# Kernel tuning notes

Measured on AMD Instinct MI355X. Metric: run time of the kernel, lower is better.

## Reference

```python
import jax, jax.numpy as jnp
import numpy as np

N_NODES = 40000
N_EDGES = 640000
N_GRAPHS = 64
D_IN = 128
D_H = 128
N_LAYERS = 3
EPS = 1e-5


def _layer_norm(x, g, b):
    mu = jnp.mean(x, axis=-1, keepdims=True)
    var = jnp.var(x, axis=-1, keepdims=True)
    return (x - mu) * jax.lax.rsqrt(var + EPS) * g + b


def _sage_conv(x, src, dst, Wl, bl, Wr):
    # mean aggregation of neighbor messages: i <- mean_{j: (j->i)} x_j
    msg = x[src]                                              # [E, d]
    agg = jax.ops.segment_sum(msg, dst, num_segments=N_NODES)  # [N, d]
    deg = jax.ops.segment_sum(jnp.ones((src.shape[0],), x.dtype), dst,
                              num_segments=N_NODES)
    agg = agg / jnp.clip(deg, 1.0)[:, None]
    # out = lin_l(agg) + lin_r(x)
    return agg @ Wl.T + bl + x @ Wr.T


def setup_inputs() -> dict:
    key = jax.random.key(0)
    ks = jax.random.split(key, 12)
    s = 0.05
    x = jax.random.normal(ks[0], (N_NODES, D_IN), jnp.float32)
    edge_index = jax.random.randint(ks[1], (2, N_EDGES), 0, N_NODES, jnp.int64)
    batch = jnp.sort(jax.random.randint(ks[2], (N_NODES,), 0, N_GRAPHS, jnp.int64))
    fc_w = jax.random.normal(ks[3], (D_H, D_IN), jnp.float32) * s
    fc_b = jax.random.normal(ks[4], (D_H,), jnp.float32) * s
    Wl = jax.random.normal(ks[5], (N_LAYERS, D_H, D_H), jnp.float32) * s
    bl = jax.random.normal(ks[6], (N_LAYERS, D_H), jnp.float32) * s
    Wr = jax.random.normal(ks[7], (N_LAYERS, D_H, D_H), jnp.float32) * s
    ln_g = jnp.ones((N_LAYERS - 1, D_H), jnp.float32)
    ln_b = jnp.zeros((N_LAYERS - 1, D_H), jnp.float32)
    return {"x": x, "edge_index": edge_index, "batch": batch,
            "fc_w": fc_w, "fc_b": fc_b, "Wl": Wl, "bl": bl, "Wr": Wr,
            "ln_g": ln_g, "ln_b": ln_b}


def reference(x, edge_index, batch, fc_w, fc_b, Wl, bl, Wr, ln_g, ln_b):
    src, dst = edge_index[0], edge_index[1]
    # input projection + ReLU
    h = jax.nn.relu(x @ fc_w.T + fc_b)
    # GraphSAGE stack: norm + ReLU between layers, none after the last
    for i in range(N_LAYERS):
        h = _sage_conv(h, src, dst, Wl[i], bl[i], Wr[i])
        if i < N_LAYERS - 1:
            h = jax.nn.relu(_layer_norm(h, ln_g[i], ln_b[i]))
    node_embed = h                                            # [N, D_H]
    graph_embed = jax.ops.segment_sum(node_embed, batch,
                                      num_segments=N_GRAPHS)  # [G, D_H]
    return node_embed, graph_embed
```

## Files before the change

### kernel.cpp

```cpp
#include <hip/hip_runtime.h>
#include <hip/hip_bf16.h>


#define N_NODES 40000
#define N_EDGES 640000
#define N_GRAPHS 64
#define D 128
#define NODE_ELEMS 5120000
#define N_TILES 1250
#define ELL_W 64

typedef __hip_bfloat16 bf16;
typedef __attribute__((ext_vector_type(8))) short bf16x8;
typedef __attribute__((ext_vector_type(4))) float f32x4;

__device__ __forceinline__ float b2f(bf16 v) { return __bfloat162float(v); }
__device__ __forceinline__ bf16 f2b(float v) { return __float2bfloat16(v); }
__device__ __forceinline__ float lo2f(unsigned w) { return __uint_as_float(w << 16); }
__device__ __forceinline__ float hi2f(unsigned w) { return __uint_as_float(w & 0xffff0000u); }
__device__ __forceinline__ unsigned packbf(float a, float b) {
    union { bf16 h[2]; unsigned u; } c;
    c.h[0] = f2b(a); c.h[1] = f2b(b);
    return c.u;
}
__device__ __forceinline__ int is_bf16(const unsigned* lng) {
    return (lng[0] == 0x3f803f80u) ? 1 : 0;
}
__device__ __forceinline__ int edge_is_i64(const void* edge) {
    const unsigned* ew = (const unsigned*)edge;
    return (ew[1] == 0u && ew[3] == 0u && ew[5] == 0u) ? 1 : 0;
}

union U8 { uint4 u; bf16x8 s; };

__device__ __forceinline__ bf16x8 load8(const void* base, long idx, int isb) {
    if (isb) {
        U8 t;
        t.u = *(const uint4*)((const bf16*)base + idx);
        return t.s;
    }
    const float* f = (const float*)base + idx;
    float4 f0 = *(const float4*)f;
    float4 f1 = *(const float4*)(f + 4);
    union { bf16 h[8]; bf16x8 s; } t;
    t.h[0] = f2b(f0.x); t.h[1] = f2b(f0.y); t.h[2] = f2b(f0.z); t.h[3] = f2b(f0.w);
    t.h[4] = f2b(f1.x); t.h[5] = f2b(f1.y); t.h[6] = f2b(f1.z); t.h[7] = f2b(f1.w);
    return t.s;
}

#define CW2_TOTAL 99200
__global__ __launch_bounds__(256, 2) void k_main(
    const void* __restrict__ X, const void* __restrict__ fcw,
    const void* __restrict__ fcb, bf16* __restrict__ outb,
    const void* __restrict__ edge, const void* __restrict__ batch,
    const void* Wl, const void* bl, const void* Wr,
    const void* lng, const void* lnb,
    int* __restrict__ cursor, unsigned short* __restrict__ ell,
    int* __restrict__ batch32, bf16* __restrict__ cw,
    float* __restrict__ gsum) {
    const int bid = blockIdx.x, t = threadIdx.x;
    int role, id;
    if (bid < 1000) { role = (bid & 1) ? 0 : 1; id = bid >> 1; }
    else if (bid < 1012) { role = 0; id = 500 + (bid - 1000); }
    else if (bid < 1169) { role = 2; id = bid - 1012; }
    else { role = 3; id = bid - 1169; }

    if (role == 1) {
        const int i64 = edge_is_i64(edge);
        int s[5], d[5];
#pragma unroll
        for (int i = 0; i < 5; i++) {
            int e = id * 1280 + i * 256 + t;
            if (i64) {
                s[i] = (int)((const long long*)edge)[e];
                d[i] = (int)((const long long*)edge)[N_EDGES + e];
            } else {
                s[i] = ((const int*)edge)[e];
                d[i] = ((const int*)edge)[N_EDGES + e];
            }
        }
        int p[5];
#pragma unroll
        for (int i = 0; i < 5; i++) p[i] = atomicAdd(&cursor[d[i]], 1);
#pragma unroll
        for (int i = 0; i < 5; i++)
            if (p[i] < ELL_W) ell[d[i] * ELL_W + p[i]] = (unsigned short)s[i];
        return;
    }
    if (role == 2) {
        int j = id * 256 + t;
        if (j < N_NODES)
            batch32[j] = edge_is_i64(edge) ? (int)((const long long*)batch)[j]
                                           : ((const int*)batch)[j];
        return;
    }
    if (role == 3) {
        int i = id * 256 + t;
        if (i >= CW2_TOTAL) return;
        int isb = is_bf16((const unsigned*)lng);
        const void* s; int o;
        if (i < 49152)       { s = Wl;  o = i; }
        else if (i < 49536)  { s = bl;  o = i - 49152; }
        else if (i < 98688)  { s = Wr;  o = i - 49536; }
        else if (i < 98944)  { s = lng; o = i - 98688; }
        else                 { s = lnb; o = i - 98944; }
        cw[i] = isb ? ((const bf16*)s)[o] : f2b(((const float*)s)[o]);
        return;
    }

    {
        int i = id * 256 + t;
        if (i < N_GRAPHS * D) gsum[i] = 0.f;
    }
    const int lane = t & 63;
    const int wave = t >> 6;
    const int n = lane & 15, q = lane >> 4;
    const int rowgrp = wave >> 1;
    const int cb = (wave & 1) * 64;
    const int isb = is_bf16((const unsigned*)lng);

    bf16x8 wf[4][4];
#pragma unroll
    for (int ct = 0; ct < 4; ct++)
#pragma unroll
        for (int ks = 0; ks < 4; ks++)
            wf[ct][ks] = load8(fcw, (long)(cb + ct * 16 + n) * 128 + ks * 32 + q * 8, isb);
    float bz[4];
#pragma unroll
    for (int ct = 0; ct < 4; ct++)
        bz[ct] = isb ? b2f(((const bf16*)fcb)[cb + ct * 16 + n])
                     : ((const float*)fcb)[cb + ct * 16 + n];

    const f32x4 zero = {0.f, 0.f, 0.f, 0.f};
    for (int tile = id; tile < N_TILES; tile += 512) {
        const long rbase = (long)tile * 32 + rowgrp * 16 + n;
        f32x4 acc[4] = {zero, zero, zero, zero};
        bf16x8 af[4];
#pragma unroll
        for (int ks = 0; ks < 4; ks++)
            af[ks] = load8(X, rbase * 128 + ks * 32 + q * 8, isb);
#pragma unroll
        for (int ct = 0; ct < 4; ct++)
#pragma unroll
            for (int ks = 0; ks < 4; ks++)
                acc[ct] = __builtin_amdgcn_mfma_f32_16x16x32_bf16(
                    af[ks], wf[ct][ks], acc[ct], 0, 0, 0);
#pragma unroll
        for (int ct = 0; ct < 4; ct++) {
            const int col = cb + ct * 16 + n;
#pragma unroll
            for (int r = 0; r < 4; r++) {
                const long row = (long)tile * 32 + rowgrp * 16 + q * 4 + r;
                outb[row * 128 + col] = f2b(fmaxf(acc[ct][r] + bz[ct], 0.f));
            }
        }
    }
}

__global__ void k_agg(const bf16* __restrict__ h, const int* __restrict__ cursor,
                      const unsigned short* __restrict__ ell, bf16* __restrict__ agg) {
    const int node = blockIdx.x * 16 + (threadIdx.x >> 4);
    const int l16 = threadIdx.x & 15;
    const int deg = min(cursor[node], ELL_W);
    const int dm1 = max(deg - 1, 0);
    const unsigned short* row = ell + node * ELL_W;
    const uint4* hp = (const uint4*)h;
    float a0 = 0.f, a1 = 0.f, a2 = 0.f, a3 = 0.f;
    float a4 = 0.f, a5 = 0.f, a6 = 0.f, a7 = 0.f;
    for (int e = 0; e < deg; e += 8) {
#pragma unroll
        for (int i = 0; i < 8; i++) {
            int ei = min(e + i, dm1);
            int idx = (int)row[ei];
            uint4 w = hp[(size_t)idx * 16 + l16];
            float m = (e + i < deg) ? 1.f : 0.f;
            a0 = fmaf(m, lo2f(w.x), a0); a1 = fmaf(m, hi2f(w.x), a1);
            a2 = fmaf(m, lo2f(w.y), a2); a3 = fmaf(m, hi2f(w.y), a3);
            a4 = fmaf(m, lo2f(w.z), a4); a5 = fmaf(m, hi2f(w.z), a5);
            a6 = fmaf(m, lo2f(w.w), a6); a7 = fmaf(m, hi2f(w.w), a7);
        }
    }
    float inv = 1.f / (float)max(deg, 1);
    uint4 o;
    o.x = packbf(a0 * inv, a1 * inv);
    o.y = packbf(a2 * inv, a3 * inv);
    o.z = packbf(a4 * inv, a5 * inv);
    o.w = packbf(a6 * inv, a7 * inv);
    ((uint4*)agg)[(size_t)node * 16 + l16] = o;
}

template <int MODE>
__global__ __launch_bounds__(256, 2) void k_gemm(
    const bf16* __restrict__ A, const bf16* __restrict__ W1,
    const bf16* __restrict__ B, const bf16* __restrict__ W2,
    const bf16* __restrict__ bias, bf16* __restrict__ outb,
    void* __restrict__ outx, const bf16* __restrict__ lgam,
    const bf16* __restrict__ lbet, const unsigned* __restrict__ lngraw) {
    __shared__ float sred[2][2][16][2];
    const int tid = threadIdx.x;
    const int lane = tid & 63;
    const int wave = tid >> 6;
    const int n = lane & 15, q = lane >> 4;
    const int rowgrp = wave >> 1;
    const int cbi = wave & 1;
    const int cb = cbi * 64;
    const int isb = is_bf16(lngraw);

    bf16x8 wf[2][4][4];
#pragma unroll
    for (int p = 0; p < 2; p++) {
        const bf16* Wp = p ? W2 : W1;
#pragma unroll
        for (int ct = 0; ct < 4; ct++)
#pragma unroll
            for (int ks = 0; ks < 4; ks++) {
                U8 t;
                t.u = *(const uint4*)&Wp[(cb + ct * 16 + n) * 128 + ks * 32 + q * 8];
                wf[p][ct][ks] = t.s;
            }
    }
    float bz[4], gf[4], bf_[4];
#pragma unroll
    for (int ct = 0; ct < 4; ct++) {
        bz[ct] = b2f(bias[cb + ct * 16 + n]);
        if (MODE == 1) {
            gf[ct] = b2f(lgam[cb + ct * 16 + n]);
            bf_[ct] = b2f(lbet[cb + ct * 16 + n]);
        }
    }

    const f32x4 zero = {0.f, 0.f, 0.f, 0.f};

    for (int tile = blockIdx.x; tile < N_TILES; tile += gridDim.x) {
        const long rbase = (long)tile * 32 + rowgrp * 16 + n;
        f32x4 acc[4] = {zero, zero, zero, zero};
#pragma unroll
        for (int p = 0; p < 2; p++) {
            const bf16* Ap = p ? B : A;
            bf16x8 af[4];
#pragma unroll
            for (int ks = 0; ks < 4; ks++) {
                U8 t;
                t.u = *(const uint4*)&Ap[rbase * 128 + ks * 32 + q * 8];
                af[ks] = t.s;
            }
#pragma unroll
            for (int ct = 0; ct < 4; ct++)
#pragma unroll
                for (int ks = 0; ks < 4; ks++)
                    acc[ct] = __builtin_amdgcn_mfma_f32_16x16x32_bf16(
                        af[ks], wf[p][ct][ks], acc[ct], 0, 0, 0);
        }

        float vs[4][4];
#pragma unroll
        for (int ct = 0; ct < 4; ct++)
#pragma unroll
            for (int r = 0; r < 4; r++) vs[ct][r] = acc[ct][r] + bz[ct];

        if (MODE == 1) {
            float s[4], ss[4];
#pragma unroll
            for (int r = 0; r < 4; r++) {
                s[r] = 0.f; ss[r] = 0.f;
#pragma unroll
                for (int ct = 0; ct < 4; ct++) {
                    s[r] += vs[ct][r];
                    ss[r] += vs[ct][r] * vs[ct][r];
                }
            }
#pragma unroll
            for (int m = 1; m <= 8; m <<= 1)
#pragma unroll
                for (int r = 0; r < 4; r++) {
                    s[r] += __shfl_xor(s[r], m, 64);
                    ss[r] += __shfl_xor(ss[r], m, 64);
                }
            if (n == 0) {
#pragma unroll
                for (int r = 0; r < 4; r++) {
                    sred[rowgrp][cbi][q * 4 + r][0] = s[r];
                    sred[rowgrp][cbi][q * 4 + r][1] = ss[r];
                }
            }
            __syncthreads();
#pragma unroll
            for (int r = 0; r < 4; r++) {
                float S = s[r] + sred[rowgrp][1 - cbi][q * 4 + r][0];
                float SS = ss[r] + sred[rowgrp][1 - cbi][q * 4 + r][1];
                float mu = S * (1.f / 128.f);
                float var = SS * (1.f / 128.f) - mu * mu;
                float rstd = rsqrtf(var + 1e-5f);
#pragma unroll
                for (int ct = 0; ct < 4; ct++)
                    vs[ct][r] = fmaxf((vs[ct][r] - mu) * rstd * gf[ct] + bf_[ct], 0.f);
            }
            __syncthreads();
        }

#pragma unroll
        for (int ct = 0; ct < 4; ct++) {
            const int col = cb + ct * 16 + n;
#pragma unroll
            for (int r = 0; r < 4; r++) {
                const long row = (long)tile * 32 + rowgrp * 16 + q * 4 + r;
                float v = vs[ct][r];
                if (MODE == 1) {
                    outb[row * 128 + col] = f2b(v);
                } else {
                    if (isb) ((bf16*)outx)[row * 128 + col] = f2b(v);
                    else ((float*)outx)[row * 128 + col] = v;
                }
            }
        }
    }
}

__device__ __forceinline__ int lbound(const int* a, int n, int key) {
    int lo = 0, hi = n;
    while (lo < hi) {
        int mid = (lo + hi) >> 1;
        if (a[mid] < key) lo = mid + 1; else hi = mid;
    }
    return lo;
}

__global__ void k_graph(const void* __restrict__ node, const int* __restrict__ batch,
                        float* __restrict__ gsum, const unsigned* __restrict__ lngraw) {
    const int g = blockIdx.x >> 4, part = blockIdx.x & 15;
    const int c = threadIdx.x;
    const int isb = is_bf16(lngraw);
    const int lo = lbound(batch, N_NODES, g);
    const int hi = lbound(batch, N_NODES, g + 1);
    const int len = hi - lo;
    const int b0 = lo + (len * part) / 16;
    const int b1 = lo + (len * (part + 1)) / 16;
    float s0 = 0.f, s1 = 0.f;
    int n = b0;
    if (isb) {
        const bf16* nb = (const bf16*)node;
        for (; n + 2 <= b1; n += 2) {
            s0 += b2f(nb[(size_t)(n + 0) * 128 + c]);
            s1 += b2f(nb[(size_t)(n + 1) * 128 + c]);
        }
        for (; n < b1; n++) s0 += b2f(nb[(size_t)n * 128 + c]);
    } else {
        const float* nf = (const float*)node;
        for (; n + 2 <= b1; n += 2) {
            s0 += nf[(size_t)(n + 0) * 128 + c];
            s1 += nf[(size_t)(n + 1) * 128 + c];
        }
        for (; n < b1; n++) s0 += nf[(size_t)n * 128 + c];
    }
    atomicAdd(&gsum[g * 128 + c], s0 + s1);
}

__global__ void k_gout(const float* __restrict__ gsum, void* __restrict__ out,
                       const unsigned* __restrict__ lngraw) {
    int i = blockIdx.x * 256 + threadIdx.x;
    if (i >= N_GRAPHS * D) return;
    if (is_bf16(lngraw)) ((bf16*)out)[NODE_ELEMS + i] = f2b(gsum[i]);
    else ((float*)out)[NODE_ELEMS + i] = gsum[i];
}

extern "C" void kernel_launch(void* const* d_in, const int* in_sizes, int n_in,
                              void* d_out, int out_size, void* d_ws, size_t ws_size,
                              hipStream_t stream) {
    const void* x = d_in[0];
    const void* edge = d_in[1];
    const void* batch = d_in[2];
    const void* fc_w = d_in[3];
    const void* fc_b = d_in[4];
    const void* Wl = d_in[5];
    const void* bl = d_in[6];
    const void* Wr = d_in[7];
    const void* ln_g = d_in[8];
    const void* ln_b = d_in[9];
    const unsigned* lngraw = (const unsigned*)ln_g;

    size_t off = 0;
    char* base = (char*)d_ws;
    auto carve = [&](size_t bytes) -> char* {
        char* p = base + off;
        off = (off + bytes + 255) & ~(size_t)255;
        return p;
    };
    bf16* cw = (bf16*)carve((size_t)CW2_TOTAL * 2);
    bf16* hA = (bf16*)carve((size_t)NODE_ELEMS * 2);
    bf16* hB = (bf16*)carve((size_t)NODE_ELEMS * 2);
    bf16* agg = (bf16*)carve((size_t)NODE_ELEMS * 2);
    int* batch32 = (int*)carve((size_t)N_NODES * 4);
    unsigned short* ell = (unsigned short*)carve((size_t)N_NODES * ELL_W * 2);
    int* cursor = (int*)carve((size_t)N_NODES * 4);
    float* gsum = (float*)carve((size_t)N_GRAPHS * D * 4);

    const bf16* cw_Wl = cw;
    const bf16* cw_bl = cw + 49152;
    const bf16* cw_Wr = cw + 49536;
    const bf16* cw_lng = cw + 98688;
    const bf16* cw_lnb = cw + 98944;

    hipMemsetAsync(cursor, 0, (size_t)N_NODES * 4, stream);
    k_main<<<1557, 256, 0, stream>>>(x, fc_w, fc_b, hA, edge, batch,
                                     Wl, bl, Wr, ln_g, ln_b,
                                     cursor, ell, batch32, cw, gsum);

    bf16* hcur = hA;
    bf16* hnext = hB;
    for (int l = 0; l < 3; l++) {
        k_agg<<<2500, 256, 0, stream>>>(hcur, cursor, ell, agg);
        const bf16* W1 = cw_Wl + (size_t)l * 16384;
        const bf16* W2 = cw_Wr + (size_t)l * 16384;
        const bf16* bb = cw_bl + (size_t)l * 128;
        if (l < 2) {
            k_gemm<1><<<512, 256, 0, stream>>>(agg, W1, hcur, W2, bb, hnext,
                                               nullptr, cw_lng + (size_t)l * 128,
                                               cw_lnb + (size_t)l * 128, lngraw);
            bf16* t = hcur; hcur = hnext; hnext = t;
        } else {
            k_gemm<2><<<512, 256, 0, stream>>>(agg, W1, hcur, W2, bb, nullptr,
                                               d_out, nullptr, nullptr, lngraw);
        }
    }

    k_graph<<<1024, 128, 0, stream>>>(d_out, batch32, gsum, lngraw);
    k_gout<<<32, 256, 0, stream>>>(gsum, d_out, lngraw);
}
```

Measured before the change: 248.2 us.

## Gather neighbor features from an FP8 e4m3 copy in aggregation

The producing kernels now also write an 8-bit e4m3-style copy of each node's hidden features alongside the bf16 copy. The neighbor-aggregation kernel gathers these 8-byte-per-lane values instead of 16-byte bf16 values and decodes them with shifts and a power-of-two rescale. This halves the bytes moved by the random gather, which is the main memory cost of mean aggregation. In exchange it adds extra byte stores in the GEMM epilogues and loses precision in the aggregated messages (3 mantissa bits, values assumed non-negative after ReLU, clamped at the top of the range).

```diff
diff --git a/kernel.cpp b/kernel.cpp
--- a/kernel.cpp
+++ b/kernel.cpp
@@ -23,6 +23,11 @@
     c.h[0] = f2b(a); c.h[1] = f2b(b);
     return c.u;
 }
+__device__ __forceinline__ unsigned char f2e4m3(float v) {
+    unsigned u = __float_as_uint(v * 0x1p-120f);
+    unsigned r = (u + 0x0007ffffu + ((u >> 20) & 1u)) >> 20;
+    return (unsigned char)min(r, 0x7eu);
+}
 __device__ __forceinline__ int is_bf16(const unsigned* lng) {
     return (lng[0] == 0x3f803f80u) ? 1 : 0;
 }
@@ -52,6 +57,7 @@
 __global__ __launch_bounds__(256, 2) void k_main(
     const void* __restrict__ X, const void* __restrict__ fcw,
     const void* __restrict__ fcb, bf16* __restrict__ outb,
+    unsigned char* __restrict__ out8,
     const void* __restrict__ edge, const void* __restrict__ batch,
     const void* Wl, const void* bl, const void* Wr,
     const void* lng, const void* lnb,
@@ -151,20 +157,24 @@
 #pragma unroll
             for (int r = 0; r < 4; r++) {
                 const long row = (long)tile * 32 + rowgrp * 16 + q * 4 + r;
-                outb[row * 128 + col] = f2b(fmaxf(acc[ct][r] + bz[ct], 0.f));
-            }
-        }
-    }
-}
-
-__global__ void k_agg(const bf16* __restrict__ h, const int* __restrict__ cursor,
-                      const unsigned short* __restrict__ ell, bf16* __restrict__ agg) {
+                float v = fmaxf(acc[ct][r] + bz[ct], 0.f);
+                outb[row * 128 + col] = f2b(v);
+                out8[row * 128 + col] = f2e4m3(v);
+            }
+        }
+    }
+}
+
+__global__ void k_agg8(const unsigned char* __restrict__ h8,
+                       const int* __restrict__ cursor,
+                       const unsigned short* __restrict__ ell,
+                       bf16* __restrict__ agg) {
     const int node = blockIdx.x * 16 + (threadIdx.x >> 4);
     const int l16 = threadIdx.x & 15;
     const int deg = min(cursor[node], ELL_W);
     const int dm1 = max(deg - 1, 0);
     const unsigned short* row = ell + node * ELL_W;
-    const uint4* hp = (const uint4*)h;
+    const uint2* hp = (const uint2*)h8;
     float a0 = 0.f, a1 = 0.f, a2 = 0.f, a3 = 0.f;
     float a4 = 0.f, a5 = 0.f, a6 = 0.f, a7 = 0.f;
     for (int e = 0; e < deg; e += 8) {
@@ -172,12 +182,16 @@
         for (int i = 0; i < 8; i++) {
             int ei = min(e + i, dm1);
             int idx = (int)row[ei];
-            uint4 w = hp[(size_t)idx * 16 + l16];
-            float m = (e + i < deg) ? 1.f : 0.f;
-            a0 = fmaf(m, lo2f(w.x), a0); a1 = fmaf(m, hi2f(w.x), a1);
-            a2 = fmaf(m, lo2f(w.y), a2); a3 = fmaf(m, hi2f(w.y), a3);
-            a4 = fmaf(m, lo2f(w.z), a4); a5 = fmaf(m, hi2f(w.z), a5);
-            a6 = fmaf(m, lo2f(w.w), a6); a7 = fmaf(m, hi2f(w.w), a7);
+            uint2 w = hp[(size_t)idx * 16 + l16];
+            const float ms = (e + i < deg) ? 0x1p120f : 0.f;
+            a0 = fmaf(ms, __uint_as_float((w.x << 20) & 0x07f00000u), a0);
+            a1 = fmaf(ms, __uint_as_float((w.x << 12) & 0x07f00000u), a1);
+            a2 = fmaf(ms, __uint_as_float((w.x << 4)  & 0x07f00000u), a2);
+            a3 = fmaf(ms, __uint_as_float((w.x >> 4)  & 0x07f00000u), a3);
+            a4 = fmaf(ms, __uint_as_float((w.y << 20) & 0x07f00000u), a4);
+            a5 = fmaf(ms, __uint_as_float((w.y << 12) & 0x07f00000u), a5);
+            a6 = fmaf(ms, __uint_as_float((w.y << 4)  & 0x07f00000u), a6);
+            a7 = fmaf(ms, __uint_as_float((w.y >> 4)  & 0x07f00000u), a7);
         }
     }
     float inv = 1.f / (float)max(deg, 1);
@@ -194,8 +208,9 @@
     const bf16* __restrict__ A, const bf16* __restrict__ W1,
     const bf16* __restrict__ B, const bf16* __restrict__ W2,
     const bf16* __restrict__ bias, bf16* __restrict__ outb,
-    void* __restrict__ outx, const bf16* __restrict__ lgam,
-    const bf16* __restrict__ lbet, const unsigned* __restrict__ lngraw) {
+    unsigned char* __restrict__ out8, void* __restrict__ outx,
+    const bf16* __restrict__ lgam, const bf16* __restrict__ lbet,
+    const unsigned* __restrict__ lngraw) {
     __shared__ float sred[2][2][16][2];
     const int tid = threadIdx.x;
     const int lane = tid & 63;
@@ -307,6 +322,7 @@
                 float v = vs[ct][r];
                 if (MODE == 1) {
                     outb[row * 128 + col] = f2b(v);
+                    out8[row * 128 + col] = f2e4m3(v);
                 } else {
                     if (isb) ((bf16*)outx)[row * 128 + col] = f2b(v);
                     else ((float*)outx)[row * 128 + col] = v;
@@ -389,6 +405,8 @@
     bf16* hA = (bf16*)carve((size_t)NODE_ELEMS * 2);
     bf16* hB = (bf16*)carve((size_t)NODE_ELEMS * 2);
     bf16* agg = (bf16*)carve((size_t)NODE_ELEMS * 2);
+    unsigned char* h8A = (unsigned char*)carve((size_t)NODE_ELEMS);
+    unsigned char* h8B = (unsigned char*)carve((size_t)NODE_ELEMS);
     int* batch32 = (int*)carve((size_t)N_NODES * 4);
     unsigned short* ell = (unsigned short*)carve((size_t)N_NODES * ELL_W * 2);
     int* cursor = (int*)carve((size_t)N_NODES * 4);
@@ -401,25 +419,30 @@
     const bf16* cw_lnb = cw + 98944;
 
     hipMemsetAsync(cursor, 0, (size_t)N_NODES * 4, stream);
-    k_main<<<1557, 256, 0, stream>>>(x, fc_w, fc_b, hA, edge, batch,
+    k_main<<<1557, 256, 0, stream>>>(x, fc_w, fc_b, hA, h8A, edge, batch,
                                      Wl, bl, Wr, ln_g, ln_b,
                                      cursor, ell, batch32, cw, gsum);
 
     bf16* hcur = hA;
     bf16* hnext = hB;
+    unsigned char* h8cur = h8A;
+    unsigned char* h8next = h8B;
     for (int l = 0; l < 3; l++) {
-        k_agg<<<2500, 256, 0, stream>>>(hcur, cursor, ell, agg);
         const bf16* W1 = cw_Wl + (size_t)l * 16384;
         const bf16* W2 = cw_Wr + (size_t)l * 16384;
         const bf16* bb = cw_bl + (size_t)l * 128;
+        k_agg8<<<2500, 256, 0, stream>>>(h8cur, cursor, ell, agg);
         if (l < 2) {
             k_gemm<1><<<512, 256, 0, stream>>>(agg, W1, hcur, W2, bb, hnext,
-                                               nullptr, cw_lng + (size_t)l * 128,
+                                               h8next, nullptr,
+                                               cw_lng + (size_t)l * 128,
                                                cw_lnb + (size_t)l * 128, lngraw);
             bf16* t = hcur; hcur = hnext; hnext = t;
+            unsigned char* t8 = h8cur; h8cur = h8next; h8next = t8;
         } else {
             k_gemm<2><<<512, 256, 0, stream>>>(agg, W1, hcur, W2, bb, nullptr,
-                                               d_out, nullptr, nullptr, lngraw);
+                                               nullptr, d_out, nullptr, nullptr,
+                                               lngraw);
         }
     }
 
```

Measured after the change: 242.2 us. 2.4% less time.
